# Kernel tuning notes

Measured on AMD Instinct MI355X. Metric: run time of the kernel, lower is better.

Reference implementation:

```python
import jax, jax.numpy as jnp
import numpy as np

N_NODES = 50000
DEG = 32
N_EDGES = N_NODES * DEG
IN_DIM = 256
HID = 64
OUT = 64
N_CLASSES = 40
N_GRAPHS = 64
NEG_SLOPE = 0.2


def setup_inputs() -> dict:
    key = jax.random.key(0)
    ks = jax.random.split(key, 12)
    h = jax.random.normal(ks[0], (N_NODES, IN_DIM), dtype=jnp.float32)
    # every node has exactly DEG incoming edges -> dst sorted, no zero in-degree
    dst = jnp.repeat(jnp.arange(N_NODES, dtype=jnp.int32), DEG)
    src = jax.random.randint(ks[1], (N_EDGES,), 0, N_NODES, dtype=jnp.int32)
    # evenly sized graphs so mean_nodes never divides by zero
    graph_ids = (jnp.arange(N_NODES, dtype=jnp.int32) * N_GRAPHS) // N_NODES
    s1 = 1.0 / np.sqrt(IN_DIM)
    s2 = 1.0 / np.sqrt(HID)
    W1 = jax.random.normal(ks[2], (IN_DIM, HID), jnp.float32) * s1
    al1 = jax.random.normal(ks[3], (HID,), jnp.float32) * s2
    ar1 = jax.random.normal(ks[4], (HID,), jnp.float32) * s2
    b1 = jnp.zeros((HID,), jnp.float32)
    W2 = jax.random.normal(ks[5], (HID, OUT), jnp.float32) * s2
    al2 = jax.random.normal(ks[6], (OUT,), jnp.float32) / np.sqrt(OUT)
    ar2 = jax.random.normal(ks[7], (OUT,), jnp.float32) / np.sqrt(OUT)
    b2 = jnp.zeros((OUT,), jnp.float32)
    p_drop = jnp.full((HID,), 0.5, jnp.float32)  # VariationalDropout retain probs
    Wc = jax.random.normal(ks[8], (OUT, N_CLASSES), jnp.float32) / np.sqrt(OUT)
    bc = jnp.zeros((N_CLASSES,), jnp.float32)
    return {"h": h, "src": src, "dst": dst, "graph_ids": graph_ids,
            "n_graphs": N_GRAPHS, "W1": W1, "al1": al1, "ar1": ar1, "b1": b1,
            "W2": W2, "al2": al2, "ar2": ar2, "b2": b2,
            "p_drop": p_drop, "Wc": Wc, "bc": bc}


def _gat_conv(h, W, al, ar, b, src, dst, n_nodes):
    f = h @ W                                  # [N, d]
    el = f @ al                                # [N]
    er = f @ ar                                # [N]
    e = jax.nn.leaky_relu(el[src] + er[dst], NEG_SLOPE)   # [E]
    m = jax.ops.segment_max(e, dst, num_segments=n_nodes, indices_are_sorted=True)
    ex = jnp.exp(e - m[dst])
    s = jax.ops.segment_sum(ex, dst, num_segments=n_nodes, indices_are_sorted=True)
    alpha = ex / s[dst]                        # edge softmax over incoming edges
    out = jax.ops.segment_sum(alpha[:, None] * f[src], dst,
                              num_segments=n_nodes, indices_are_sorted=True)
    return out + b


def reference(h, src, dst, graph_ids, n_graphs, W1, al1, ar1, b1,
              W2, al2, ar2, b2, p_drop, Wc, bc):
    n_nodes = h.shape[0]
    x = jax.nn.elu(_gat_conv(h, W1, al1, ar1, b1, src, dst, n_nodes))
    x = x * jnp.clip(p_drop, 0.0, 1.0)[None, :]          # deterministic var-dropout
    x = _gat_conv(x, W2, al2, ar2, b2, src, dst, n_nodes)
    # dgl.mean_nodes
    sums = jax.ops.segment_sum(x, graph_ids, num_segments=n_graphs, indices_are_sorted=True)
    cnts = jax.ops.segment_sum(jnp.ones((n_nodes,), x.dtype), graph_ids,
                               num_segments=n_graphs, indices_are_sorted=True)
    hg = sums / cnts[:, None]
    return hg @ Wc + bc
```

## Files before the change

### kernel.cpp

```cpp
#include <hip/hip_runtime.h>
#include <hip/hip_bf16.h>

#define N_NODES   50000
#define DEG       32
#define IN_DIM    256
#define HID       64
#define OUTD      64
#define N_CLASSES 40
#define N_GRAPHS  64

typedef __attribute__((ext_vector_type(8))) short bf16x8;
typedef __attribute__((ext_vector_type(4))) float f32x4;

__device__ __forceinline__ unsigned short f2bf(float f) {
  unsigned int u = __float_as_uint(f);
  return (unsigned short)((u + 0x7fffu + ((u >> 16) & 1u)) >> 16);
}

__device__ __forceinline__ unsigned int f2bf2(float lo, float hi) {
  return (unsigned int)f2bf(lo) | ((unsigned int)f2bf(hi) << 16);
}

__device__ __forceinline__ float2 bf2_to_f2(unsigned int v) {
  float2 r;
  r.x = __uint_as_float(v << 16);
  r.y = __uint_as_float(v & 0xffff0000u);
  return r;
}

template<int K_DIM, typename AT = float>
__global__ __launch_bounds__(256)
void gemm_heads_mfma(const AT* __restrict__ A, const float* __restrict__ W,
                     const float* __restrict__ al, const float* __restrict__ ar,
                     unsigned short* __restrict__ Fb, float* __restrict__ el,
                     float* __restrict__ er, int n_rows)
{
  constexpr int KP = K_DIM + 8;
  __shared__ __align__(16) unsigned short Wt[64 * KP];

  {
    constexpr int ITER = K_DIM * 64 / 1024;
    #pragma unroll
    for (int i = 0; i < ITER; ++i) {
      const int idx4 = threadIdx.x * 4 + i * 1024;
      const int k = idx4 >> 6;
      const int c = idx4 & 63;
      const float4 w = *reinterpret_cast<const float4*>(&W[idx4]);
      Wt[(c + 0) * KP + k] = f2bf(w.x);
      Wt[(c + 1) * KP + k] = f2bf(w.y);
      Wt[(c + 2) * KP + k] = f2bf(w.z);
      Wt[(c + 3) * KP + k] = f2bf(w.w);
    }
  }
  __syncthreads();

  const int lane = threadIdx.x & 63;
  const int wv   = threadIdx.x >> 6;
  const int c    = lane & 15;
  const int g    = lane >> 4;
  const int row0 = blockIdx.x * 64 + wv * 16;

  const long arow = min(row0 + c, n_rows - 1);
  const int  kq   = g * 8;

  f32x4 acc[4];
  #pragma unroll
  for (int nt = 0; nt < 4; ++nt) acc[nt] = (f32x4){0.f, 0.f, 0.f, 0.f};

  #pragma unroll
  for (int ks = 0; ks < K_DIM / 32; ++ks) {
    bf16x8 afv;
    if constexpr (sizeof(AT) == 4) {
      const float4 q0 = *reinterpret_cast<const float4*>(&A[arow * K_DIM + ks * 32 + kq]);
      const float4 q1 = *reinterpret_cast<const float4*>(&A[arow * K_DIM + ks * 32 + kq + 4]);
      union { bf16x8 v; unsigned short u[8]; } af;
      af.u[0] = f2bf(q0.x); af.u[1] = f2bf(q0.y); af.u[2] = f2bf(q0.z); af.u[3] = f2bf(q0.w);
      af.u[4] = f2bf(q1.x); af.u[5] = f2bf(q1.y); af.u[6] = f2bf(q1.z); af.u[7] = f2bf(q1.w);
      afv = af.v;
    } else {
      afv = *reinterpret_cast<const bf16x8*>(&A[arow * K_DIM + ks * 32 + kq]);
    }
    #pragma unroll
    for (int nt = 0; nt < 4; ++nt) {
      const bf16x8 bf =
          *reinterpret_cast<const bf16x8*>(&Wt[(nt * 16 + c) * KP + ks * 32 + kq]);
      acc[nt] = __builtin_amdgcn_mfma_f32_16x16x32_bf16(afv, bf, acc[nt], 0, 0, 0);
    }
  }

  #pragma unroll
  for (int nt = 0; nt < 4; ++nt) {
    #pragma unroll
    for (int r = 0; r < 4; ++r) {
      const int row = row0 + g * 4 + r;
      if (row < n_rows) Fb[(long)row * 64 + nt * 16 + c] = f2bf(acc[nt][r]);
    }
  }

  float alc[4], arc[4];
  #pragma unroll
  for (int nt = 0; nt < 4; ++nt) { alc[nt] = al[nt * 16 + c]; arc[nt] = ar[nt * 16 + c]; }

  float pe[4], pr[4];
  #pragma unroll
  for (int r = 0; r < 4; ++r) {
    pe[r] = acc[0][r] * alc[0] + acc[1][r] * alc[1] + acc[2][r] * alc[2] + acc[3][r] * alc[3];
    pr[r] = acc[0][r] * arc[0] + acc[1][r] * arc[1] + acc[2][r] * arc[2] + acc[3][r] * arc[3];
  }
  #pragma unroll
  for (int d = 1; d < 16; d <<= 1) {
    #pragma unroll
    for (int r = 0; r < 4; ++r) {
      pe[r] += __shfl_xor(pe[r], d);
      pr[r] += __shfl_xor(pr[r], d);
    }
  }
  if (c == 0) {
    #pragma unroll
    for (int r = 0; r < 4; ++r) {
      const int row = row0 + g * 4 + r;
      if (row < n_rows) { el[row] = pe[r]; er[row] = pr[r]; }
    }
  }
}

template<int MODE>
__global__ __launch_bounds__(256)
void agg_kernel(const unsigned int* __restrict__ F2,
                const float* __restrict__ el, const float* __restrict__ er,
                const int* __restrict__ src, const float* __restrict__ bias,
                const float* __restrict__ pd, void* __restrict__ Xout, int n_pairs)
{
  __shared__ int   sS[4][64];
  __shared__ float sA[4][64];

  const int tid  = threadIdx.x;
  const int wv   = tid >> 6;
  const int lane = tid & 63;
  const int wid  = (blockIdx.x * 256 + tid) >> 6;
  if (wid >= n_pairs) return;

  const int half = lane >> 5;
  const int node = wid * 2 + half;
  const int q    = lane & 7;
  const int e8   = lane >> 3;

  const int s = src[wid * 64 + lane];
  sS[wv][lane] = s;

  int sv[8];
  #pragma unroll
  for (int t = 0; t < 8; ++t) sv[t] = sS[wv][t * 8 + e8];

  const uint4* __restrict__ FP = reinterpret_cast<const uint4*>(F2);
  const uint4 v0 = FP[(long)sv[0] * 8 + q];
  const uint4 v1 = FP[(long)sv[1] * 8 + q];
  const uint4 v2 = FP[(long)sv[2] * 8 + q];
  const uint4 v3 = FP[(long)sv[3] * 8 + q];
  const uint4 v4 = FP[(long)sv[4] * 8 + q];
  const uint4 v5 = FP[(long)sv[5] * 8 + q];
  const uint4 v6 = FP[(long)sv[6] * 8 + q];
  const uint4 v7 = FP[(long)sv[7] * 8 + q];

  float ev = el[s] + er[node];
  ev = ev > 0.f ? ev : 0.2f * ev;
  float m = ev;
  #pragma unroll
  for (int d = 16; d; d >>= 1) m = fmaxf(m, __shfl_xor(m, d));
  const float p = __expf(ev - m);
  float sum = p;
  #pragma unroll
  for (int d = 16; d; d >>= 1) sum += __shfl_xor(sum, d);

  sA[wv][lane] = p / sum;
  float av[8];
  #pragma unroll
  for (int t = 0; t < 8; ++t) av[t] = sA[wv][t * 8 + e8];

  float accA[8], accB[8];
  #pragma unroll
  for (int j = 0; j < 8; ++j) { accA[j] = 0.f; accB[j] = 0.f; }

  auto consume = [&](const uint4& vv, float a, float* acc) {
    const float2 f0 = bf2_to_f2(vv.x);
    const float2 f1 = bf2_to_f2(vv.y);
    const float2 f2 = bf2_to_f2(vv.z);
    const float2 f3 = bf2_to_f2(vv.w);
    acc[0] = fmaf(a, f0.x, acc[0]);
    acc[1] = fmaf(a, f0.y, acc[1]);
    acc[2] = fmaf(a, f1.x, acc[2]);
    acc[3] = fmaf(a, f1.y, acc[3]);
    acc[4] = fmaf(a, f2.x, acc[4]);
    acc[5] = fmaf(a, f2.y, acc[5]);
    acc[6] = fmaf(a, f3.x, acc[6]);
    acc[7] = fmaf(a, f3.y, acc[7]);
  };
  consume(v0, av[0], accA);
  consume(v1, av[1], accA);
  consume(v2, av[2], accA);
  consume(v3, av[3], accA);
  consume(v4, av[4], accB);
  consume(v5, av[5], accB);
  consume(v6, av[6], accB);
  consume(v7, av[7], accB);

  #pragma unroll
  for (int d = 8; d < 64; d <<= 1) {
    #pragma unroll
    for (int j = 0; j < 8; ++j) {
      accA[j] += __shfl_xor(accA[j], d);
      accB[j] += __shfl_xor(accB[j], d);
    }
  }

  if ((e8 & 3) == 0) {
    const float* accp = half ? accB : accA;
    const int wnode = wid * 2 + half;
    float o[8];
    #pragma unroll
    for (int j = 0; j < 8; ++j) {
      const int col = q * 8 + j;
      float v = accp[j] + bias[col];
      if (MODE == 1) {
        v = v > 0.f ? v : (__expf(v) - 1.f);
        v *= fminf(fmaxf(pd[col], 0.f), 1.f);
      }
      o[j] = v;
    }
    if (MODE == 1) {
      uint4 pk;
      pk.x = f2bf2(o[0], o[1]);
      pk.y = f2bf2(o[2], o[3]);
      pk.z = f2bf2(o[4], o[5]);
      pk.w = f2bf2(o[6], o[7]);
      *reinterpret_cast<uint4*>(
          &((unsigned short*)Xout)[(long)wnode * 64 + q * 8]) = pk;
    } else {
      float4* dst = reinterpret_cast<float4*>(&((float*)Xout)[(long)wnode * 64 + q * 8]);
      dst[0] = make_float4(o[0], o[1], o[2], o[3]);
      dst[1] = make_float4(o[4], o[5], o[6], o[7]);
    }
  }
}

__global__ __launch_bounds__(256)
void partial_pool_kernel(const float* __restrict__ X2, float* __restrict__ sums)
{
  const int wv   = (blockIdx.x * 256 + threadIdx.x) >> 6;
  const int lane = threadIdx.x & 63;
  if (wv >= N_NODES / 16) return;
  const int base = wv * 16;

  float accR = 0.f;
  int   gcur = (base * 64) / N_NODES;
  #pragma unroll 4
  for (int n = 0; n < 16; ++n) {
    const int i = base + n;
    const int g = (i * 64) / N_NODES;
    if (g != gcur) {
      atomicAdd(&sums[gcur * 64 + lane], accR);
      accR = 0.f; gcur = g;
    }
    accR += X2[(long)i * 64 + lane];
  }
  atomicAdd(&sums[gcur * 64 + lane], accR);
}

__global__ __launch_bounds__(64)
void classify_kernel(const float* __restrict__ sums, const float* __restrict__ Wc,
                     const float* __restrict__ bc, float* __restrict__ out)
{
  const int g     = blockIdx.x;
  const int start = (g * N_NODES + N_GRAPHS - 1) / N_GRAPHS;
  const int end   = ((g + 1) * N_NODES + N_GRAPHS - 1) / N_GRAPHS;
  const int t     = threadIdx.x;

  __shared__ float hg[64];
  hg[t] = sums[g * 64 + t] / (float)(end - start);
  __syncthreads();
  if (t < N_CLASSES) {
    float o = bc[t];
    #pragma unroll
    for (int j = 0; j < 64; ++j) o = fmaf(hg[j], Wc[j * N_CLASSES + t], o);
    out[g * N_CLASSES + t] = o;
  }
}

extern "C" void kernel_launch(void* const* d_in, const int* in_sizes, int n_in,
                              void* d_out, int out_size, void* d_ws, size_t ws_size,
                              hipStream_t stream)
{
  const float* h   = (const float*)d_in[0];
  const int*   src = (const int*)d_in[1];
  const float* W1  = (const float*)d_in[5];
  const float* al1 = (const float*)d_in[6];
  const float* ar1 = (const float*)d_in[7];
  const float* b1  = (const float*)d_in[8];
  const float* W2  = (const float*)d_in[9];
  const float* al2 = (const float*)d_in[10];
  const float* ar2 = (const float*)d_in[11];
  const float* b2  = (const float*)d_in[12];
  const float* pd  = (const float*)d_in[13];
  const float* Wc  = (const float*)d_in[14];
  const float* bc  = (const float*)d_in[15];
  float* out = (float*)d_out;

  float*          ws   = (float*)d_ws;
  float*          xbuf = ws;
  unsigned short* Fb   = (unsigned short*)(ws + 3200000);
  unsigned short* Xb   = (unsigned short*)(ws + 4800000);
  float*          elb  = ws + 6400000;
  float*          erb  = elb + 50000;
  float*          sums = erb + 50000;

  hipMemsetAsync(sums, 0, N_GRAPHS * 64 * sizeof(float), stream);

  gemm_heads_mfma<IN_DIM, float><<<(N_NODES + 63) / 64, 256, 0, stream>>>(
      h, W1, al1, ar1, Fb, elb, erb, N_NODES);
  agg_kernel<1><<<(N_NODES / 2) / 4, 256, 0, stream>>>(
      (const unsigned int*)Fb, elb, erb, src, b1, pd, (void*)Xb, N_NODES / 2);

  gemm_heads_mfma<HID, unsigned short><<<(N_NODES + 63) / 64, 256, 0, stream>>>(
      Xb, W2, al2, ar2, Fb, elb, erb, N_NODES);
  agg_kernel<2><<<(N_NODES / 2) / 4, 256, 0, stream>>>(
      (const unsigned int*)Fb, elb, erb, src, b2, pd, (void*)xbuf, N_NODES / 2);

  partial_pool_kernel<<<(N_NODES / 16 + 3) / 4, 256, 0, stream>>>(xbuf, sums);
  classify_kernel<<<N_GRAPHS, 64, 0, stream>>>(sums, Wc, bc, out);
}
```

Baseline: 194.5 us.

## Fuse mean-pool partial sums into layer-2 aggregation and drop memset

The layer-2 aggregation kernel now puts each node's biased output into shared memory. One wave then reduces the block's 8 nodes per graph and atomically adds them into the per-graph sums. This removes the full fp32 node-feature write and read-back and the separate pooling kernel launch. The hipMemsetAsync is replaced by block 0 of each GEMM kernel zeroing the sums buffer. The cost is about twice as many global atomics and an extra block-level barrier in the aggregation kernel.

```diff
diff --git a/kernel.cpp b/kernel.cpp
--- a/kernel.cpp
+++ b/kernel.cpp
@@ -33,8 +33,13 @@
 void gemm_heads_mfma(const AT* __restrict__ A, const float* __restrict__ W,
                      const float* __restrict__ al, const float* __restrict__ ar,
                      unsigned short* __restrict__ Fb, float* __restrict__ el,
-                     float* __restrict__ er, int n_rows)
+                     float* __restrict__ er, float* __restrict__ sums, int n_rows)
 {
+  if (blockIdx.x == 0) {
+    #pragma unroll
+    for (int i = 0; i < 16; ++i) sums[threadIdx.x + 256 * i] = 0.f;
+  }
+
   constexpr int KP = K_DIM + 8;
   __shared__ __align__(16) unsigned short Wt[64 * KP];
 
@@ -133,6 +138,7 @@
 {
   __shared__ int   sS[4][64];
   __shared__ float sA[4][64];
+  __shared__ float sX[8][64];
 
   const int tid  = threadIdx.x;
   const int wv   = tid >> 6;
@@ -213,21 +219,19 @@
     }
   }
 
-  if ((e8 & 3) == 0) {
-    const float* accp = half ? accB : accA;
-    const int wnode = wid * 2 + half;
-    float o[8];
-    #pragma unroll
-    for (int j = 0; j < 8; ++j) {
-      const int col = q * 8 + j;
-      float v = accp[j] + bias[col];
-      if (MODE == 1) {
+  if (MODE == 1) {
+    if ((e8 & 3) == 0) {
+      const float* accp = half ? accB : accA;
+      const int wnode = wid * 2 + half;
+      float o[8];
+      #pragma unroll
+      for (int j = 0; j < 8; ++j) {
+        const int col = q * 8 + j;
+        float v = accp[j] + bias[col];
         v = v > 0.f ? v : (__expf(v) - 1.f);
         v *= fminf(fmaxf(pd[col], 0.f), 1.f);
+        o[j] = v;
       }
-      o[j] = v;
-    }
-    if (MODE == 1) {
       uint4 pk;
       pk.x = f2bf2(o[0], o[1]);
       pk.y = f2bf2(o[2], o[3]);
@@ -235,35 +239,33 @@
       pk.w = f2bf2(o[6], o[7]);
       *reinterpret_cast<uint4*>(
           &((unsigned short*)Xout)[(long)wnode * 64 + q * 8]) = pk;
-    } else {
-      float4* dst = reinterpret_cast<float4*>(&((float*)Xout)[(long)wnode * 64 + q * 8]);
-      dst[0] = make_float4(o[0], o[1], o[2], o[3]);
-      dst[1] = make_float4(o[4], o[5], o[6], o[7]);
-    }
-  }
-}
-
-__global__ __launch_bounds__(256)
-void partial_pool_kernel(const float* __restrict__ X2, float* __restrict__ sums)
-{
-  const int wv   = (blockIdx.x * 256 + threadIdx.x) >> 6;
-  const int lane = threadIdx.x & 63;
-  if (wv >= N_NODES / 16) return;
-  const int base = wv * 16;
-
-  float accR = 0.f;
-  int   gcur = (base * 64) / N_NODES;
-  #pragma unroll 4
-  for (int n = 0; n < 16; ++n) {
-    const int i = base + n;
-    const int g = (i * 64) / N_NODES;
-    if (g != gcur) {
-      atomicAdd(&sums[gcur * 64 + lane], accR);
-      accR = 0.f; gcur = g;
-    }
-    accR += X2[(long)i * 64 + lane];
-  }
-  atomicAdd(&sums[gcur * 64 + lane], accR);
+    }
+  } else {
+    if ((e8 & 3) == 0) {
+      const float* accp = half ? accB : accA;
+      const int slot = wv * 2 + half;
+      #pragma unroll
+      for (int j = 0; j < 8; ++j)
+        sX[slot][q * 8 + j] = accp[j] + bias[q * 8 + j];
+    }
+    __syncthreads();
+    if (tid < 64) {
+      float* sums = (float*)Xout;
+      const int base = blockIdx.x * 8;
+      float acc = 0.f;
+      int gcur = (base * 64) / N_NODES;
+      #pragma unroll
+      for (int n = 0; n < 8; ++n) {
+        const int g = ((base + n) * 64) / N_NODES;
+        if (g != gcur) {
+          atomicAdd(&sums[gcur * 64 + tid], acc);
+          acc = 0.f; gcur = g;
+        }
+        acc += sX[n][tid];
+      }
+      atomicAdd(&sums[gcur * 64 + tid], acc);
+    }
+  }
 }
 
 __global__ __launch_bounds__(64)
@@ -306,25 +308,21 @@
   float* out = (float*)d_out;
 
   float*          ws   = (float*)d_ws;
-  float*          xbuf = ws;
   unsigned short* Fb   = (unsigned short*)(ws + 3200000);
   unsigned short* Xb   = (unsigned short*)(ws + 4800000);
   float*          elb  = ws + 6400000;
   float*          erb  = elb + 50000;
   float*          sums = erb + 50000;
 
-  hipMemsetAsync(sums, 0, N_GRAPHS * 64 * sizeof(float), stream);
-
   gemm_heads_mfma<IN_DIM, float><<<(N_NODES + 63) / 64, 256, 0, stream>>>(
-      h, W1, al1, ar1, Fb, elb, erb, N_NODES);
+      h, W1, al1, ar1, Fb, elb, erb, sums, N_NODES);
   agg_kernel<1><<<(N_NODES / 2) / 4, 256, 0, stream>>>(
       (const unsigned int*)Fb, elb, erb, src, b1, pd, (void*)Xb, N_NODES / 2);
 
   gemm_heads_mfma<HID, unsigned short><<<(N_NODES + 63) / 64, 256, 0, stream>>>(
-      Xb, W2, al2, ar2, Fb, elb, erb, N_NODES);
+      Xb, W2, al2, ar2, Fb, elb, erb, sums, N_NODES);
   agg_kernel<2><<<(N_NODES / 2) / 4, 256, 0, stream>>>(
-      (const unsigned int*)Fb, elb, erb, src, b2, pd, (void*)xbuf, N_NODES / 2);
-
-  partial_pool_kernel<<<(N_NODES / 16 + 3) / 4, 256, 0, stream>>>(xbuf, sums);
+      (const unsigned int*)Fb, elb, erb, src, b2, pd, (void*)sums, N_NODES / 2);
+
   classify_kernel<<<N_GRAPHS, 64, 0, stream>>>(sums, Wc, bc, out);
 }
```

After: 188.6 us. 1.03x faster.
